# Kernel tuning notes

Measured on AMD Instinct MI355X. Metric: run time of the kernel, lower is better.

The kernel has to match this reference:

```python
import jax, jax.numpy as jnp
import numpy as np

B, T, D, H = 4, 1024, 1024, 16
HD = D // H
EPS = 1e-5


def setup_inputs() -> dict:
    key = jax.random.key(0)
    ks = jax.random.split(key, 8)
    input_tensor = jax.random.normal(ks[0], (B, T, D), dtype=jnp.float32)
    # contiguous valid prefixes (realistic padding mask); True = valid
    lengths = jax.random.randint(ks[1], (B,), T // 2, T + 1)
    sequence_mask = jnp.arange(T)[None, :] < lengths[:, None]
    # online attention mask: causal (True = position allowed)
    attn_mask = jnp.tril(jnp.ones((T, T), dtype=bool))
    scale = 1.0 / np.sqrt(D)
    in_proj_w = jax.random.normal(ks[2], (3 * D, D), dtype=jnp.float32) * scale
    in_proj_b = jnp.zeros((3 * D,), dtype=jnp.float32)
    out_w = jax.random.normal(ks[3], (D, D), dtype=jnp.float32) * scale
    out_b = jnp.zeros((D,), dtype=jnp.float32)
    ln_gamma = jnp.ones((D,), dtype=jnp.float32)
    ln_beta = jnp.zeros((D,), dtype=jnp.float32)
    return {
        "input_tensor": input_tensor,
        "ln_gamma": ln_gamma,
        "ln_beta": ln_beta,
        "in_proj_w": in_proj_w,
        "in_proj_b": in_proj_b,
        "out_w": out_w,
        "out_b": out_b,
        "sequence_mask": sequence_mask,
        "attn_mask": attn_mask,
    }


def reference(input_tensor, ln_gamma, ln_beta, in_proj_w, in_proj_b, out_w, out_b,
              sequence_mask, attn_mask):
    # LayerNorm over last dim
    mu = jnp.mean(input_tensor, axis=-1, keepdims=True)
    var = jnp.mean(jnp.square(input_tensor - mu), axis=-1, keepdims=True)
    x = (input_tensor - mu) * jax.lax.rsqrt(var + EPS) * ln_gamma + ln_beta

    # shared QKV projection (torch MHA packed in_proj)
    qkv = x @ in_proj_w.T + in_proj_b  # [B,T,3D]
    q, k, v = jnp.split(qkv, 3, axis=-1)
    q = q.reshape(B, T, H, HD) * (1.0 / np.sqrt(HD))
    k = k.reshape(B, T, H, HD)
    v = v.reshape(B, T, H, HD)

    scores = jnp.einsum("bqhd,bkhd->bhqk", q, k)  # [B,H,T,T], shared

    keypad = sequence_mask[:, None, None, :]          # True = valid key
    online_ok = keypad & attn_mask[None, None, :, :]  # padding + attn mask
    neg_inf = jnp.float32(-jnp.inf)

    def attend(ok_mask):
        p = jax.nn.softmax(jnp.where(ok_mask, scores, neg_inf), axis=-1)
        o = jnp.einsum("bhqk,bkhd->bqhd", p, v).reshape(B, T, D)
        return o @ out_w.T + out_b

    out_online = attend(online_ok)   # key_padding + attn_mask
    out_offline = attend(keypad)     # key_padding only (full context)
    # training path: cat on dim 0 then view(2, B, T, D)
    return jnp.stack((out_online, out_offline), axis=0)
```

## Files before the change

kernel.cpp:

```cpp
#include <hip/hip_runtime.h>

#define B_ 4
#define T_ 1024
#define D_ 1024
#define H_ 16
#define HD_ 64

typedef unsigned short u16;
typedef __bf16 bf16x8 __attribute__((ext_vector_type(8)));
typedef float f32x4 __attribute__((ext_vector_type(4)));
typedef unsigned short u16x4 __attribute__((ext_vector_type(4)));

__device__ inline u16 f2b(float f) {
    union { float f; unsigned u; } v; v.f = f;
    unsigned r = v.u + 0x7fffu + ((v.u >> 16) & 1u);
    return (u16)(r >> 16);
}

__device__ inline f32x4 mfma16(bf16x8 a, bf16x8 b, f32x4 c) {
    return __builtin_amdgcn_mfma_f32_16x16x32_bf16(a, b, c, 0, 0, 0);
}

__global__ __launch_bounds__(256) void prep_ln_kernel(
    const float* __restrict__ x, const float* __restrict__ g,
    const float* __restrict__ be, u16* __restrict__ y,
    const float* __restrict__ wqkv_f, u16* __restrict__ wqkv,
    const float* __restrict__ wo_f, u16* __restrict__ wo,
    const unsigned char* __restrict__ m, int* __restrict__ lens) {
    const int blk = blockIdx.x;
    const int tid = threadIdx.x;
    if (blk < 4096) {
        __shared__ float red[8];
        const float* xr = x + (size_t)blk * D_;
        float4 v = ((const float4*)xr)[tid];
        float s  = v.x + v.y + v.z + v.w;
        float ss = v.x*v.x + v.y*v.y + v.z*v.z + v.w*v.w;
#pragma unroll
        for (int off = 1; off < 64; off <<= 1) {
            s  += __shfl_xor(s, off);
            ss += __shfl_xor(ss, off);
        }
        const int w = tid >> 6;
        if ((tid & 63) == 0) { red[w*2] = s; red[w*2+1] = ss; }
        __syncthreads();
        s  = red[0] + red[2] + red[4] + red[6];
        ss = red[1] + red[3] + red[5] + red[7];
        const float mu = s * (1.f/1024.f);
        const float rs = rsqrtf(ss*(1.f/1024.f) - mu*mu + 1e-5f);
        float4 gv = ((const float4*)g)[tid];
        float4 bv = ((const float4*)be)[tid];
        u16x4 o = { f2b((v.x-mu)*rs*gv.x + bv.x),
                    f2b((v.y-mu)*rs*gv.y + bv.y),
                    f2b((v.z-mu)*rs*gv.z + bv.z),
                    f2b((v.w-mu)*rs*gv.w + bv.w) };
        ((u16x4*)(y + (size_t)blk * D_))[tid] = o;
    } else if (blk < 5120) {
        const int n4 = (3 * D_ * D_) / 4;
        for (int i = (blk - 4096) * 256 + tid; i < n4; i += 1024 * 256) {
            float4 v = ((const float4*)wqkv_f)[i];
            u16x4 o = { f2b(v.x), f2b(v.y), f2b(v.z), f2b(v.w) };
            ((u16x4*)wqkv)[i] = o;
        }
    } else if (blk < 5632) {
        const int n4 = (D_ * D_) / 4;
        for (int i = (blk - 5120) * 256 + tid; i < n4; i += 512 * 256) {
            float4 v = ((const float4*)wo_f)[i];
            u16x4 o = { f2b(v.x), f2b(v.y), f2b(v.z), f2b(v.w) };
            ((u16x4*)wo)[i] = o;
        }
    } else {
        const int b = blk - 5632;
        const int esz4 = (m[1] == 0);
        int c = 0;
        for (int i = tid; i < T_; i += 256) {
            bool v = esz4 ? (((const int*)m)[b * T_ + i] != 0) : (m[b * T_ + i] != 0);
            c += v ? 1 : 0;
        }
#pragma unroll
        for (int off = 1; off < 64; off <<= 1) c += __shfl_xor(c, off);
        __shared__ int redi[4];
        if ((tid & 63) == 0) redi[tid >> 6] = c;
        __syncthreads();
        if (tid == 0) lens[b] = redi[0] + redi[1] + redi[2] + redi[3];
    }
}

template <int EPI, int SWAP>
__global__ __launch_bounds__(256) void gemm_bt(
    const u16* __restrict__ A, const u16* __restrict__ Bw,
    const float* __restrict__ bias, float* __restrict__ Cf,
    u16* __restrict__ Qb, u16* __restrict__ Kb, u16* __restrict__ Vt,
    int M, int N, int K) {
    __shared__ u16 As[2][128 * 64];
    __shared__ u16 Bs[2][128 * 64];
    const int tid = threadIdx.x;
    const int w = tid >> 6, l = tid & 63;
    const int l15 = l & 15, lg = l >> 4;
    const int m0 = (SWAP ? blockIdx.x : blockIdx.y) * 128;
    const int n0 = (SWAP ? blockIdx.y : blockIdx.x) * 128;
    const int wr = w >> 1, wc = w & 1;
    const int srow = l >> 3;
    const int scg  = (l & 7) ^ srow;
    const int swa  = l15 & 7;

    const int lin = blockIdx.y * gridDim.x + blockIdx.x;
    if (lin & 256) __builtin_amdgcn_s_sleep(24);

    f32x4 acc[4][4];
#pragma unroll
    for (int m = 0; m < 4; m++)
#pragma unroll
        for (int n = 0; n < 4; n++) acc[m][n] = (f32x4){0.f, 0.f, 0.f, 0.f};

    const int KS = K >> 6;

    auto stage = [&](int buf, int ks) {
        const int k0 = ks * 64;
#pragma unroll
        for (int it = 0; it < 4; ++it) {
            const int c = it * 4 + w;
            const int row = c * 8 + srow;
            const u16* ga = A  + (size_t)(m0 + row) * K + (k0 + scg * 8);
            const u16* gb = Bw + (size_t)(n0 + row) * K + (k0 + scg * 8);
            __builtin_amdgcn_global_load_lds(
                (const __attribute__((address_space(1))) unsigned int*)ga,
                (__attribute__((address_space(3))) unsigned int*)(&As[buf][c * 512]), 16, 0, 0);
            __builtin_amdgcn_global_load_lds(
                (const __attribute__((address_space(1))) unsigned int*)gb,
                (__attribute__((address_space(3))) unsigned int*)(&Bs[buf][c * 512]), 16, 0, 0);
        }
    };

    stage(0, 0);

    int buf = 0;
    for (int ks = 0; ks < KS; ++ks) {
        if (ks + 1 < KS) {
            stage(buf ^ 1, ks + 1);
            asm volatile("s_waitcnt vmcnt(8)" ::: "memory");
        } else {
            asm volatile("s_waitcnt vmcnt(0)" ::: "memory");
        }
        __builtin_amdgcn_sched_barrier(0);
        __builtin_amdgcn_s_barrier();
        __builtin_amdgcn_sched_barrier(0);
#pragma unroll
        for (int h = 0; h < 2; ++h) {
            bf16x8 af[4], bfr[4];
#pragma unroll
            for (int m = 0; m < 4; m++)
                af[m] = *(const bf16x8*)&As[buf][(wr*64 + m*16 + l15) * 64 + ((h*4 + lg) ^ swa) * 8];
#pragma unroll
            for (int n = 0; n < 4; n++)
                bfr[n] = *(const bf16x8*)&Bs[buf][(wc*64 + n*16 + l15) * 64 + ((h*4 + lg) ^ swa) * 8];
#pragma unroll
            for (int m = 0; m < 4; m++)
#pragma unroll
                for (int n = 0; n < 4; n++)
                    acc[m][n] = mfma16(af[m], bfr[n], acc[m][n]);
        }
        __builtin_amdgcn_sched_barrier(0);
        __builtin_amdgcn_s_barrier();
        __builtin_amdgcn_sched_barrier(0);
        buf ^= 1;
    }

#pragma unroll
    for (int m = 0; m < 4; m++) {
#pragma unroll
        for (int n = 0; n < 4; n++) {
            const int col = n0 + wc*64 + n*16 + l15;
            const float bv = bias[col];
            if constexpr (EPI == 0) {
#pragma unroll
                for (int r = 0; r < 4; r++) {
                    const int row = m0 + wr*64 + m*16 + lg*4 + r;
                    Cf[(size_t)row * N + col] = acc[m][n][r] + bv;
                }
            } else {
                const int which = col >> 10;
                const int d = col & 1023;
                const int h = d >> 6, hd = d & 63;
#pragma unroll
                for (int r = 0; r < 4; r++) {
                    const int row = m0 + wr*64 + m*16 + lg*4 + r;
                    const int bb = row >> 10, t = row & 1023;
                    const float v = acc[m][n][r] + bv;
                    const size_t bh = (size_t)bb * H_ + h;
                    if (which == 0)      Qb[(bh * T_ + t) * HD_ + hd] = f2b(v * 0.125f);
                    else if (which == 1) Kb[(bh * T_ + t) * HD_ + hd] = f2b(v);
                    else                 Vt[(bh * HD_ + hd) * T_ + t] = f2b(v);
                }
            }
        }
    }
}

__global__ __launch_bounds__(256) void attn_kernel(
    const u16* __restrict__ Qb, const u16* __restrict__ Kb,
    const u16* __restrict__ Vt, const int* __restrict__ lens,
    u16* __restrict__ Ob) {
    __shared__ u16 Ks[2][64 * 64];
    __shared__ u16 Vs[2][64 * 64];
    __shared__ char Pl[4][2048];
    const int qt  = blockIdx.x;
    const int bh  = blockIdx.y;
    const int b = bh >> 4, h = bh & 15;
    const int tid = threadIdx.x, w = tid >> 6, l = tid & 63;
    const int l15 = l & 15, lg = l >> 4;
    const int len = lens[b];

    const u16* Qh = Qb + (size_t)bh * (T_ * HD_);
    const u16* Kh = Kb + (size_t)bh * (T_ * HD_);
    const u16* Vh = Vt + (size_t)bh * (HD_ * T_);

    const int q0 = qt * 64 + w * 16;
    const int qrow = q0 + l15;

    const bf16x8 qf0 = *(const bf16x8*)(Qh + (size_t)qrow * HD_ + lg * 8);
    const bf16x8 qf1 = *(const bf16x8*)(Qh + (size_t)qrow * HD_ + 32 + lg * 8);

    f32x4 acc0[4], acc1[4];
#pragma unroll
    for (int n = 0; n < 4; n++) {
        acc0[n] = (f32x4){0.f, 0.f, 0.f, 0.f};
        acc1[n] = (f32x4){0.f, 0.f, 0.f, 0.f};
    }
    float l0p = 0.f, l1p = 0.f;

    const int ntk = (len + 63) >> 6;

    char* Pw = &Pl[w][0];
    const int swz = (l15 & 7) << 4;
    const int rsw = l15 & 7;

    const int srow = l >> 3;
    const int scg  = (l & 7) ^ srow;

    const float C1 = 1.44269504f, C0 = -28.8539008f;

    auto stage = [&](int buf, int kt) {
        const int k0 = kt * 64;
#pragma unroll
        for (int c = 0; c < 2; ++c) {
            const int row = (w*2 + c)*8 + srow;
            const u16* gk = Kh + (size_t)(k0 + row) * HD_ + scg*8;
            const u16* gv = Vh + (size_t)row * T_ + k0 + scg*8;
            __builtin_amdgcn_global_load_lds(
                (const __attribute__((address_space(1))) unsigned int*)gk,
                (__attribute__((address_space(3))) unsigned int*)(&Ks[buf][(w*2+c)*512]), 16, 0, 0);
            __builtin_amdgcn_global_load_lds(
                (const __attribute__((address_space(1))) unsigned int*)gv,
                (__attribute__((address_space(3))) unsigned int*)(&Vs[buf][(w*2+c)*512]), 16, 0, 0);
        }
    };

    stage(0, 0);
    __syncthreads();

    int buf = 0;
    for (int kt = 0; kt < ntk; ++kt) {
        if (kt + 1 < ntk) stage(buf ^ 1, kt + 1);
        const int k0 = kt * 64;
        const u16* Kt = &Ks[buf][0];
        const u16* Vl = &Vs[buf][0];

        f32x4 s[4];
#pragma unroll
        for (int n = 0; n < 4; n++) {
            const u16* kr = Kt + (n*16 + l15) * 64;
            bf16x8 kf0 = *(const bf16x8*)&kr[((0 + lg) ^ rsw) * 8];
            bf16x8 kf1 = *(const bf16x8*)&kr[((4 + lg) ^ rsw) * 8];
            f32x4 z = (f32x4){0.f, 0.f, 0.f, 0.f};
            z = mfma16(kf0, qf0, z);
            z = mfma16(kf1, qf1, z);
            s[n] = z;
        }
        bf16x8 vf[4][2];
#pragma unroll
        for (int n = 0; n < 4; n++) {
            const u16* vr = Vl + (n*16 + l15) * 64;
            vf[n][0] = *(const bf16x8*)&vr[((0 + lg) ^ rsw) * 8];
            vf[n][1] = *(const bf16x8*)&vr[((4 + lg) ^ rsw) * 8];
        }
        float pn = 0.f;
#pragma unroll
        for (int n = 0; n < 4; n++) {
            const int kb = k0 + n*16 + lg*4;
#pragma unroll
            for (int r = 0; r < 4; r++) {
                const float e = (kb + r < len) ? exp2f(s[n][r]*C1 + C0) : 0.f;
                s[n][r] = e;
                pn += e;
            }
        }
        const bool diag = (kt == qt);
        if (diag) {
            l0p = l1p;
#pragma unroll
            for (int n = 0; n < 4; n++) acc0[n] = acc1[n];
        }
        l1p += pn;
#pragma unroll
        for (int n = 0; n < 4; n++) {
            u16x4 pk = { f2b(s[n][0]), f2b(s[n][1]), f2b(s[n][2]), f2b(s[n][3]) };
            *(u16x4*)(Pw + ((l15*128 + n*32 + lg*8) ^ swz)) = pk;
        }
#pragma unroll
        for (int kk = 0; kk < 2; ++kk) {
            bf16x8 pa = *(const bf16x8*)(Pw + ((l15*128 + kk*64 + lg*16) ^ swz));
#pragma unroll
            for (int n = 0; n < 4; n++)
                acc1[n] = mfma16(vf[n][kk], pa, acc1[n]);
        }
        if (diag) {
            float pn0 = 0.f;
#pragma unroll
            for (int n = 0; n < 4; n++) {
                const int kb = k0 + n*16 + lg*4;
#pragma unroll
                for (int r = 0; r < 4; r++) {
                    const float e = (kb + r <= qrow) ? s[n][r] : 0.f;
                    s[n][r] = e;
                    pn0 += e;
                }
            }
            l0p += pn0;
#pragma unroll
            for (int n = 0; n < 4; n++) {
                u16x4 pk = { f2b(s[n][0]), f2b(s[n][1]), f2b(s[n][2]), f2b(s[n][3]) };
                *(u16x4*)(Pw + ((l15*128 + n*32 + lg*8) ^ swz)) = pk;
            }
#pragma unroll
            for (int kk = 0; kk < 2; ++kk) {
                bf16x8 pa = *(const bf16x8*)(Pw + ((l15*128 + kk*64 + lg*16) ^ swz));
#pragma unroll
                for (int n = 0; n < 4; n++)
                    acc0[n] = mfma16(vf[n][kk], pa, acc0[n]);
            }
        }
        __syncthreads();
        buf ^= 1;
    }

    if (qt >= ntk) {
        l0p = l1p;
#pragma unroll
        for (int n = 0; n < 4; n++) acc0[n] = acc1[n];
    }

    float l0 = l0p + __shfl_xor(l0p, 16);
    l0 += __shfl_xor(l0, 32);
    float l1 = l1p + __shfl_xor(l1p, 16);
    l1 += __shfl_xor(l1, 32);

    const float inv0 = 1.f / l0;
    const float inv1 = 1.f / l1;
    u16* O0 = Ob + ((size_t)b * T_ + qrow) * D_ + h * HD_;
    u16* O1 = O0 + (size_t)B_ * T_ * D_;
#pragma unroll
    for (int n = 0; n < 4; n++) {
        u16x4 o0 = { f2b(acc0[n][0] * inv0), f2b(acc0[n][1] * inv0),
                     f2b(acc0[n][2] * inv0), f2b(acc0[n][3] * inv0) };
        u16x4 o1 = { f2b(acc1[n][0] * inv1), f2b(acc1[n][1] * inv1),
                     f2b(acc1[n][2] * inv1), f2b(acc1[n][3] * inv1) };
        *(u16x4*)(O0 + n*16 + lg*4) = o0;
        *(u16x4*)(O1 + n*16 + lg*4) = o1;
    }
}

extern "C" void kernel_launch(void* const* d_in, const int* in_sizes, int n_in,
                              void* d_out, int out_size, void* d_ws, size_t ws_size,
                              hipStream_t stream) {
    const float* x_in   = (const float*)d_in[0];
    const float* gamma  = (const float*)d_in[1];
    const float* beta   = (const float*)d_in[2];
    const float* wqkv_f = (const float*)d_in[3];
    const float* bqkv   = (const float*)d_in[4];
    const float* wout_f = (const float*)d_in[5];
    const float* bout   = (const float*)d_in[6];
    const unsigned char* smask = (const unsigned char*)d_in[7];
    float* out = (float*)d_out;

    char* ws = (char*)d_ws;
    u16* xb   = (u16*)(ws);
    u16* wqkv = (u16*)(ws + ((size_t)8  << 20));
    u16* wo   = (u16*)(ws + ((size_t)14 << 20));
    u16* Qb   = (u16*)(ws + ((size_t)16 << 20));
    u16* Kb   = (u16*)(ws + ((size_t)24 << 20));
    u16* Vt   = (u16*)(ws + ((size_t)32 << 20));
    u16* Ob   = (u16*)(ws + ((size_t)40 << 20));
    int* lens = (int*)(ws + ((size_t)56 << 20));

    prep_ln_kernel<<<dim3(5636), dim3(256), 0, stream>>>(
        x_in, gamma, beta, xb, wqkv_f, wqkv, wout_f, wo, smask, lens);
    gemm_bt<1, 0><<<dim3(24, 32), dim3(256), 0, stream>>>(
        xb, wqkv, bqkv, nullptr, Qb, Kb, Vt, B_ * T_, 3 * D_, D_);
    attn_kernel<<<dim3(T_ / 64, B_ * H_), dim3(256), 0, stream>>>(Qb, Kb, Vt, lens, Ob);
    gemm_bt<0, 1><<<dim3(64, 8), dim3(256), 0, stream>>>(
        Ob, wo, bout, out, nullptr, nullptr, nullptr, 2 * B_ * T_, D_, D_);
}
```

Baseline: 137.4 us.

## Replace LDS-direct double buffering with register-staged single-buffer GEMM pipeline

The GEMM mainloop no longer uses global_load_lds into a double-buffered LDS tile. It prefetches the next K-slice into registers while computing on a single LDS buffer, then writes the registers to LDS between two barriers. This halves LDS usage, which may raise occupancy, and removes the staggered s_sleep on half the blocks. In exchange it adds VGPR pressure, an extra barrier per iteration, and explicit VMEM-to-register-to-LDS copies.

```diff
diff --git a/kernel.cpp b/kernel.cpp
--- a/kernel.cpp
+++ b/kernel.cpp
@@ -91,8 +91,8 @@
     const float* __restrict__ bias, float* __restrict__ Cf,
     u16* __restrict__ Qb, u16* __restrict__ Kb, u16* __restrict__ Vt,
     int M, int N, int K) {
-    __shared__ u16 As[2][128 * 64];
-    __shared__ u16 Bs[2][128 * 64];
+    __shared__ u16 As[128 * 64];
+    __shared__ u16 Bs[128 * 64];
     const int tid = threadIdx.x;
     const int w = tid >> 6, l = tid & 63;
     const int l15 = l & 15, lg = l >> 4;
@@ -103,9 +103,6 @@
     const int scg  = (l & 7) ^ srow;
     const int swa  = l15 & 7;
 
-    const int lin = blockIdx.y * gridDim.x + blockIdx.x;
-    if (lin & 256) __builtin_amdgcn_s_sleep(24);
-
     f32x4 acc[4][4];
 #pragma unroll
     for (int m = 0; m < 4; m++)
@@ -114,55 +111,61 @@
 
     const int KS = K >> 6;
 
-    auto stage = [&](int buf, int ks) {
+    float4 ra[4], rb[4];
+    auto loadregs = [&](int ks) {
         const int k0 = ks * 64;
 #pragma unroll
         for (int it = 0; it < 4; ++it) {
             const int c = it * 4 + w;
             const int row = c * 8 + srow;
-            const u16* ga = A  + (size_t)(m0 + row) * K + (k0 + scg * 8);
-            const u16* gb = Bw + (size_t)(n0 + row) * K + (k0 + scg * 8);
-            __builtin_amdgcn_global_load_lds(
-                (const __attribute__((address_space(1))) unsigned int*)ga,
-                (__attribute__((address_space(3))) unsigned int*)(&As[buf][c * 512]), 16, 0, 0);
-            __builtin_amdgcn_global_load_lds(
-                (const __attribute__((address_space(1))) unsigned int*)gb,
-                (__attribute__((address_space(3))) unsigned int*)(&Bs[buf][c * 512]), 16, 0, 0);
+            ra[it] = *(const float4*)(A  + (size_t)(m0 + row) * K + (k0 + scg * 8));
+            rb[it] = *(const float4*)(Bw + (size_t)(n0 + row) * K + (k0 + scg * 8));
         }
     };
-
-    stage(0, 0);
-
-    int buf = 0;
+    auto writelds = [&]() {
+#pragma unroll
+        for (int it = 0; it < 4; ++it) {
+            const int c = it * 4 + w;
+            *(float4*)((char*)As + c * 1024 + l * 16) = ra[it];
+            *(float4*)((char*)Bs + c * 1024 + l * 16) = rb[it];
+        }
+    };
+
+    loadregs(0);
+    writelds();
+    asm volatile("s_waitcnt lgkmcnt(0)" ::: "memory");
+    __builtin_amdgcn_sched_barrier(0);
+    __builtin_amdgcn_s_barrier();
+
     for (int ks = 0; ks < KS; ++ks) {
-        if (ks + 1 < KS) {
-            stage(buf ^ 1, ks + 1);
-            asm volatile("s_waitcnt vmcnt(8)" ::: "memory");
-        } else {
-            asm volatile("s_waitcnt vmcnt(0)" ::: "memory");
-        }
-        __builtin_amdgcn_sched_barrier(0);
-        __builtin_amdgcn_s_barrier();
+        if (ks + 1 < KS) loadregs(ks + 1);
         __builtin_amdgcn_sched_barrier(0);
 #pragma unroll
         for (int h = 0; h < 2; ++h) {
             bf16x8 af[4], bfr[4];
 #pragma unroll
             for (int m = 0; m < 4; m++)
-                af[m] = *(const bf16x8*)&As[buf][(wr*64 + m*16 + l15) * 64 + ((h*4 + lg) ^ swa) * 8];
+                af[m] = *(const bf16x8*)&As[(wr*64 + m*16 + l15) * 64 + ((h*4 + lg) ^ swa) * 8];
 #pragma unroll
             for (int n = 0; n < 4; n++)
-                bfr[n] = *(const bf16x8*)&Bs[buf][(wc*64 + n*16 + l15) * 64 + ((h*4 + lg) ^ swa) * 8];
+                bfr[n] = *(const bf16x8*)&Bs[(wc*64 + n*16 + l15) * 64 + ((h*4 + lg) ^ swa) * 8];
 #pragma unroll
             for (int m = 0; m < 4; m++)
 #pragma unroll
                 for (int n = 0; n < 4; n++)
                     acc[m][n] = mfma16(af[m], bfr[n], acc[m][n]);
         }
-        __builtin_amdgcn_sched_barrier(0);
-        __builtin_amdgcn_s_barrier();
-        __builtin_amdgcn_sched_barrier(0);
-        buf ^= 1;
+        if (ks + 1 < KS) {
+            asm volatile("s_waitcnt lgkmcnt(0)" ::: "memory");
+            __builtin_amdgcn_sched_barrier(0);
+            __builtin_amdgcn_s_barrier();
+            __builtin_amdgcn_sched_barrier(0);
+            writelds();
+            asm volatile("s_waitcnt lgkmcnt(0)" ::: "memory");
+            __builtin_amdgcn_sched_barrier(0);
+            __builtin_amdgcn_s_barrier();
+            __builtin_amdgcn_sched_barrier(0);
+        }
     }
 
 #pragma unroll
```

Result: slower. 250.1 us (+82.0%).

## Split QKV GEMM into dedicated 128x256 single-buffered kernel

Applied to the files above, without the earlier changes.

The QKV projection gets its own kernel with a 128x256 output tile per block, so 384 blocks replace 768. Each wave computes an 8x4 grid of MFMA tiles covering 128 rows by 64 columns, and LDS is single-buffered with plain syncthreads. The s_sleep staggering hack is dropped from both GEMMs. The larger tile raises the reuse of A loads, but it loses the double-buffered overlap of loads with compute and uses more accumulator registers, which may lower occupancy.

```diff
diff --git a/kernel.cpp b/kernel.cpp
--- a/kernel.cpp
+++ b/kernel.cpp
@@ -85,26 +85,105 @@
     }
 }
 
-template <int EPI, int SWAP>
-__global__ __launch_bounds__(256) void gemm_bt(
+__global__ __launch_bounds__(256) void gemm_qkv(
+    const u16* __restrict__ A, const u16* __restrict__ Bw,
+    const float* __restrict__ bias,
+    u16* __restrict__ Qb, u16* __restrict__ Kb, u16* __restrict__ Vt,
+    int M, int N, int K) {
+    __shared__ u16 As[128 * 64];
+    __shared__ u16 Bs[256 * 64];
+    const int tid = threadIdx.x;
+    const int w = tid >> 6, l = tid & 63;
+    const int l15 = l & 15, lg = l >> 4;
+    const int m0 = blockIdx.y * 128;
+    const int n0 = blockIdx.x * 256;
+    const int srow = l >> 3;
+    const int scg  = (l & 7) ^ srow;
+    const int swa  = l15 & 7;
+
+    f32x4 acc[8][4];
+#pragma unroll
+    for (int m = 0; m < 8; m++)
+#pragma unroll
+        for (int n = 0; n < 4; n++) acc[m][n] = (f32x4){0.f, 0.f, 0.f, 0.f};
+
+    const int KS = K >> 6;
+
+    for (int ks = 0; ks < KS; ++ks) {
+        const int k0 = ks * 64;
+#pragma unroll
+        for (int it = 0; it < 4; ++it) {
+            const int c = w * 4 + it;
+            const u16* ga = A + (size_t)(m0 + c * 8 + srow) * K + (k0 + scg * 8);
+            __builtin_amdgcn_global_load_lds(
+                (const __attribute__((address_space(1))) unsigned int*)ga,
+                (__attribute__((address_space(3))) unsigned int*)(As + c * 512), 16, 0, 0);
+        }
+#pragma unroll
+        for (int it = 0; it < 8; ++it) {
+            const int c = w * 8 + it;
+            const u16* gb = Bw + (size_t)(n0 + c * 8 + srow) * K + (k0 + scg * 8);
+            __builtin_amdgcn_global_load_lds(
+                (const __attribute__((address_space(1))) unsigned int*)gb,
+                (__attribute__((address_space(3))) unsigned int*)(Bs + c * 512), 16, 0, 0);
+        }
+        __syncthreads();
+#pragma unroll
+        for (int h = 0; h < 2; ++h) {
+            bf16x8 af[8], bfr[4];
+#pragma unroll
+            for (int n = 0; n < 4; n++)
+                bfr[n] = *(const bf16x8*)&Bs[(w*64 + n*16 + l15) * 64 + ((h*4 + lg) ^ swa) * 8];
+#pragma unroll
+            for (int m = 0; m < 8; m++)
+                af[m] = *(const bf16x8*)&As[(m*16 + l15) * 64 + ((h*4 + lg) ^ swa) * 8];
+#pragma unroll
+            for (int m = 0; m < 8; m++)
+#pragma unroll
+                for (int n = 0; n < 4; n++)
+                    acc[m][n] = mfma16(af[m], bfr[n], acc[m][n]);
+        }
+        __syncthreads();
+    }
+
+#pragma unroll
+    for (int m = 0; m < 8; m++) {
+#pragma unroll
+        for (int n = 0; n < 4; n++) {
+            const int col = n0 + w*64 + n*16 + l15;
+            const float bv = bias[col];
+            const int which = col >> 10;
+            const int d = col & 1023;
+            const int hh = d >> 6, hd = d & 63;
+#pragma unroll
+            for (int r = 0; r < 4; r++) {
+                const int row = m0 + m*16 + lg*4 + r;
+                const int bb = row >> 10, t = row & 1023;
+                const float v = acc[m][n][r] + bv;
+                const size_t bh = (size_t)bb * H_ + hh;
+                if (which == 0)      Qb[(bh * T_ + t) * HD_ + hd] = f2b(v * 0.125f);
+                else if (which == 1) Kb[(bh * T_ + t) * HD_ + hd] = f2b(v);
+                else                 Vt[(bh * HD_ + hd) * T_ + t] = f2b(v);
+            }
+        }
+    }
+}
+
+__global__ __launch_bounds__(256) void gemm_out(
     const u16* __restrict__ A, const u16* __restrict__ Bw,
     const float* __restrict__ bias, float* __restrict__ Cf,
-    u16* __restrict__ Qb, u16* __restrict__ Kb, u16* __restrict__ Vt,
     int M, int N, int K) {
     __shared__ u16 As[2][128 * 64];
     __shared__ u16 Bs[2][128 * 64];
     const int tid = threadIdx.x;
     const int w = tid >> 6, l = tid & 63;
     const int l15 = l & 15, lg = l >> 4;
-    const int m0 = (SWAP ? blockIdx.x : blockIdx.y) * 128;
-    const int n0 = (SWAP ? blockIdx.y : blockIdx.x) * 128;
+    const int m0 = blockIdx.x * 128;
+    const int n0 = blockIdx.y * 128;
     const int wr = w >> 1, wc = w & 1;
     const int srow = l >> 3;
     const int scg  = (l & 7) ^ srow;
     const int swa  = l15 & 7;
-
-    const int lin = blockIdx.y * gridDim.x + blockIdx.x;
-    if (lin & 256) __builtin_amdgcn_s_sleep(24);
 
     f32x4 acc[4][4];
 #pragma unroll
@@ -171,26 +250,10 @@
         for (int n = 0; n < 4; n++) {
             const int col = n0 + wc*64 + n*16 + l15;
             const float bv = bias[col];
-            if constexpr (EPI == 0) {
-#pragma unroll
-                for (int r = 0; r < 4; r++) {
-                    const int row = m0 + wr*64 + m*16 + lg*4 + r;
-                    Cf[(size_t)row * N + col] = acc[m][n][r] + bv;
-                }
-            } else {
-                const int which = col >> 10;
-                const int d = col & 1023;
-                const int h = d >> 6, hd = d & 63;
-#pragma unroll
-                for (int r = 0; r < 4; r++) {
-                    const int row = m0 + wr*64 + m*16 + lg*4 + r;
-                    const int bb = row >> 10, t = row & 1023;
-                    const float v = acc[m][n][r] + bv;
-                    const size_t bh = (size_t)bb * H_ + h;
-                    if (which == 0)      Qb[(bh * T_ + t) * HD_ + hd] = f2b(v * 0.125f);
-                    else if (which == 1) Kb[(bh * T_ + t) * HD_ + hd] = f2b(v);
-                    else                 Vt[(bh * HD_ + hd) * T_ + t] = f2b(v);
-                }
+#pragma unroll
+            for (int r = 0; r < 4; r++) {
+                const int row = m0 + wr*64 + m*16 + lg*4 + r;
+                Cf[(size_t)row * N + col] = acc[m][n][r] + bv;
             }
         }
     }
@@ -394,9 +457,9 @@
 
     prep_ln_kernel<<<dim3(5636), dim3(256), 0, stream>>>(
         x_in, gamma, beta, xb, wqkv_f, wqkv, wout_f, wo, smask, lens);
-    gemm_bt<1, 0><<<dim3(24, 32), dim3(256), 0, stream>>>(
-        xb, wqkv, bqkv, nullptr, Qb, Kb, Vt, B_ * T_, 3 * D_, D_);
+    gemm_qkv<<<dim3(12, 32), dim3(256), 0, stream>>>(
+        xb, wqkv, bqkv, Qb, Kb, Vt, B_ * T_, 3 * D_, D_);
     attn_kernel<<<dim3(T_ / 64, B_ * H_), dim3(256), 0, stream>>>(Qb, Kb, Vt, lens, Ob);
-    gemm_bt<0, 1><<<dim3(64, 8), dim3(256), 0, stream>>>(
-        Ob, wo, bout, out, nullptr, nullptr, nullptr, 2 * B_ * T_, D_, D_);
-}
+    gemm_out<<<dim3(64, 8), dim3(256), 0, stream>>>(
+        Ob, wo, bout, out, 2 * B_ * T_, D_, D_);
+}
```

Result: slower. 161.0 us (+17.2%).
